# Kernel optimization log

Measured on AMD Instinct MI355X. Metric: run time of the kernel, lower is better.

Reference implementation:

```python
import jax, jax.numpy as jnp
import numpy as np

B, N, D, U = 128, 1024, 16, 128


def setup_inputs() -> dict:
    key = jax.random.key(0)
    ks = jax.random.split(key, 12)
    # get_normalized_adj: D^{-1/2} (A + I) D^{-1/2} on a sparse random graph
    A = (jax.random.uniform(ks[0], (N, N)) < 0.01).astype(jnp.float32)
    A = A + jnp.eye(N, dtype=jnp.float32)
    dinv = 1.0 / jnp.sqrt(A.sum(axis=1))
    support = dinv[:, None] * A * dinv[None, :]
    s = 0.05
    return {
        "x": jax.random.normal(ks[1], (2, B, N, D), jnp.float32),
        "hx": jax.random.normal(ks[2], (B, N * U), jnp.float32),
        "delta": jax.random.normal(ks[3], (B, N, D), jnp.float32),
        "support": support,
        "kernel_r": jax.random.normal(ks[4], (D + U, 2 * U), jnp.float32) * jnp.sqrt(2.0 / (D + U)),
        "kernel_c": jax.random.normal(ks[5], (D + U, U), jnp.float32) * jnp.sqrt(2.0 / (D + U)),
        "w_out": jax.random.normal(ks[6], (U + D, D), jnp.float32) * s,
        "b_out": jax.random.normal(ks[7], (D,), jnp.float32) * s,
        "w_basis": jax.random.normal(ks[8], (D, D), jnp.float32) * s,
        "b_basis": jax.random.normal(ks[9], (D,), jnp.float32) * s,
        "lam": jax.random.normal(ks[10], (1,), jnp.float32),
    }


def reference(x, hx, delta, support, kernel_r, kernel_c, w_out, b_out, w_basis, b_basis, lam):
    y_basis, y_res = x[0], x[1]                       # (B, N, D) each
    # speculative delta (add=True branch)
    delta_value = jax.nn.relu(y_res @ w_basis + b_basis)
    p_t = jax.nn.sigmoid(y_res + 0.5 * jnp.sqrt(jnp.abs(delta + 1e-9)))
    new_delta = lam * (2.0 * p_t - 1.0) * delta_value  # (B, N, D)

    hx3 = hx.reshape(B, N, U)

    def gconv(inp, state, kernel):
        # inp (B,N,D), state (B,N,U); diffusion_step == 1 Chebyshev pass
        xs = jnp.concatenate([inp, state], axis=-1)      # (B, N, D+U)
        xs = jnp.einsum('ij,bjl->bil', support, xs)      # diffusion over nodes
        return xs @ kernel                               # (B, N, out)

    value = jax.nn.sigmoid(gconv(y_basis, hx3, kernel_r))  # (B, N, 2U)
    r, u = value[..., :U], value[..., U:]
    c = jnp.tanh(gconv(y_basis, r * hx3, kernel_c))        # (B, N, U)

    u_flat = u.reshape(B, N * U)
    c_flat = c.reshape(B, N * U)
    new_state = hx * u_flat + c_flat * (1.0 - u_flat)      # (B, N*U)

    concat = jnp.concatenate([new_state.reshape(B, N, U), y_basis], axis=-1)
    o = concat @ w_out + b_out + new_delta                 # (B, N, D)
    return (o, new_state, new_delta)
```

## Files before the change

### kernel.cpp

```cpp
#include <hip/hip_runtime.h>
#include <cstdint>

#define B_ 128
#define N_ 1024
#define D_ 16
#define U_ 128
#define M_ (B_*N_)
#define K_ 144
#define KP 192
#define CAP 48

typedef unsigned short u16;
typedef unsigned int   u32;
typedef __attribute__((ext_vector_type(8))) short bf16x8;
typedef __attribute__((ext_vector_type(4))) float f32x4;

__device__ __forceinline__ float bf2f(u16 h){ return __uint_as_float(((u32)h) << 16); }
__device__ __forceinline__ u16 f2bf(float f){
    u32 u = __float_as_uint(f);
    return (u16)((u + 0x7FFFu + ((u >> 16) & 1u)) >> 16);
}
__device__ __forceinline__ float sig_(float x){ return 1.0f / (1.0f + __expf(-x)); }

__global__ void k_ell(const float* __restrict__ sup, float* __restrict__ vals,
                      int* __restrict__ cols, int* __restrict__ nnz)
{
    int wid  = (blockIdx.x * blockDim.x + threadIdx.x) >> 6;
    int lane = threadIdx.x & 63;
    if (wid >= N_) return;
    const float* row = sup + (size_t)wid * N_;
    int base = 0;
    for (int step = 0; step < N_/64; ++step){
        int j = step*64 + lane;
        float v = row[j];
        unsigned long long m = __ballot(v != 0.0f);
        int pos = base + __popcll(m & ((1ull << lane) - 1ull));
        if (v != 0.0f && pos < CAP){ vals[wid*CAP + pos] = v; cols[wid*CAP + pos] = j; }
        base += __popcll(m);
    }
    int cnt = base < CAP ? base : CAP;
    for (int p = cnt + lane; p < CAP; p += 64){
        vals[wid*CAP + p] = 0.0f;
        cols[wid*CAP + p] = 0;
    }
    if (lane == 0) nnz[wid] = (cnt + 3) & ~3;
}

__global__ void k_prep(const float* __restrict__ kr, const float* __restrict__ kc,
                       u16* __restrict__ wr_t, u16* __restrict__ wc_t)
{
    int t = blockIdx.x * 256 + threadIdx.x;
    if (t < 256*KP){
        int col = t / KP, k = t % KP;
        wr_t[t] = f2bf(k < K_ ? kr[k*256 + col] : 0.0f);
    } else {
        int q = t - 256*KP;
        int col = q / KP, k = q % KP;
        wc_t[q] = f2bf(k < K_ ? kc[k*128 + col] : 0.0f);
    }
}


#define GQB(JJ, WW)                                                            \
    {   uint2 hh = *(const uint2*)(s16 + (int)(JJ)*16 + cq*4);                 \
        float f0 = __uint_as_float(hh.x << 16);                                \
        float f1 = __uint_as_float(hh.x & 0xFFFF0000u);                        \
        float f2 = __uint_as_float(hh.y << 16);                                \
        float f3 = __uint_as_float(hh.y & 0xFFFF0000u);                        \
        acc.x = fmaf((WW), f0, acc.x); acc.y = fmaf((WW), f1, acc.y);          \
        acc.z = fmaf((WW), f2, acc.z); acc.w = fmaf((WW), f3, acc.w); }

#define GB(T0)                                                                 \
    {   float4 wv = *(const float4*)(vt + (T0));                               \
        int4   jv = *(const int4*)(ct + (T0));                                 \
        GQB(jv.x, wv.x); GQB(jv.y, wv.y); GQB(jv.z, wv.z); GQB(jv.w, wv.w); }

#define PACK8(PK, VA, VB)                                                      \
    uint4 PK; PK.x = (u32)f2bf((VA).x) | ((u32)f2bf((VA).y) << 16);            \
    PK.y = (u32)f2bf((VA).z) | ((u32)f2bf((VA).w) << 16);                      \
    PK.z = (u32)f2bf((VB).x) | ((u32)f2bf((VB).y) << 16);                      \
    PK.w = (u32)f2bf((VB).z) | ((u32)f2bf((VB).w) << 16);

__global__ __launch_bounds__(512, 8) void k_spmm1(
        const float* __restrict__ x, const float* __restrict__ hx,
        const float* __restrict__ vals, const int* __restrict__ cols,
        const int* __restrict__ nnz, u16* __restrict__ agg)
{
    __shared__ u16 s16[1024*16];
    const int chunk = blockIdx.x;
    const int b     = blockIdx.y;
    const int tid   = threadIdx.x;
    const int cb    = chunk * 16;

    for (int q = tid; q < 2048; q += 512){
        int row = q >> 1, part = q & 1;
        const float* src = (chunk == 0)
            ? &x[((size_t)((b<<10)+row))*16 + part*8]
            : &hx[((size_t)((b<<10)+row))*128 + (cb-16) + part*8];
        float4 va = *(const float4*)src;
        float4 vb = *(const float4*)(src + 4);
        PACK8(pk, va, vb)
        *(uint4*)(s16 + row*16 + part*8) = pk;
    }
    __syncthreads();

    for (int p = tid; p < 4096; p += 512){
        int node = p >> 2, cq = p & 3;
        int c = nnz[node];
        const float* vt = vals + node*CAP;
        const int*   ct = cols + node*CAP;
        float4 acc = make_float4(0.f,0.f,0.f,0.f);
        GB(0) GB(4) GB(8) GB(12)
        for (int t0 = 16; t0 < c; t0 += 4) GB(t0)
        size_t m = (size_t)(b<<10) + node;
        ushort4 pv; pv.x = f2bf(acc.x); pv.y = f2bf(acc.y);
        pv.z = f2bf(acc.z); pv.w = f2bf(acc.w);
        *(ushort4*)&agg[m*KP + cb + cq*4] = pv;
    }
}

__global__ __launch_bounds__(512, 8) void k_spmm2(
        const u16* __restrict__ value, const float* __restrict__ hx,
        const float* __restrict__ vals, const int* __restrict__ cols,
        const int* __restrict__ nnz, u16* __restrict__ agg)
{
    __shared__ u16 s16[1024*16];
    const int chunk = blockIdx.x;
    const int b     = blockIdx.y;
    const int tid   = threadIdx.x;
    const int cb    = chunk * 16;

    for (int q = tid; q < 2048; q += 512){
        int row = q >> 1, part = q & 1;
        size_t nb = (size_t)((b<<10)+row);
        int hxcol = cb + part*8;
        float4 h0 = *(const float4*)&hx[nb*128 + hxcol];
        float4 h1 = *(const float4*)&hx[nb*128 + hxcol + 4];
        ushort4 r0 = *(const ushort4*)&value[nb*256 + hxcol];
        ushort4 r1 = *(const ushort4*)&value[nb*256 + hxcol + 4];
        float4 va = make_float4(bf2f(r0.x)*h0.x, bf2f(r0.y)*h0.y,
                                bf2f(r0.z)*h0.z, bf2f(r0.w)*h0.w);
        float4 vb = make_float4(bf2f(r1.x)*h1.x, bf2f(r1.y)*h1.y,
                                bf2f(r1.z)*h1.z, bf2f(r1.w)*h1.w);
        PACK8(pk, va, vb)
        *(uint4*)(s16 + row*16 + part*8) = pk;
    }
    __syncthreads();

    for (int p = tid; p < 4096; p += 512){
        int node = p >> 2, cq = p & 3;
        int c = nnz[node];
        const float* vt = vals + node*CAP;
        const int*   ct = cols + node*CAP;
        float4 acc = make_float4(0.f,0.f,0.f,0.f);
        GB(0) GB(4) GB(8) GB(12)
        for (int t0 = 16; t0 < c; t0 += 4) GB(t0)
        size_t m = (size_t)(b<<10) + node;
        ushort4 pv; pv.x = f2bf(acc.x); pv.y = f2bf(acc.y);
        pv.z = f2bf(acc.z); pv.w = f2bf(acc.w);
        *(ushort4*)&agg[m*KP + D_ + cb + cq*4] = pv;
    }
}


#define GEMM_STAGE_A                                                           \
    _Pragma("unroll")                                                          \
    for (int i = 0; i < 4; ++i){                                               \
        int q = tid + i*256;                                                   \
        int r_ = q >> 3, sl = q & 7;                                           \
        uint4 v = {0,0,0,0};                                                   \
        if (kb + sl*8 < K_)                                                    \
            v = *(const uint4*)(agg + (size_t)(rb+r_)*KP + kb + sl*8);         \
        *(uint4*)(a_s + r_*72 + sl*8) = v;                                     \
    }

#define GEMM_STAGE_W                                                           \
    _Pragma("unroll")                                                          \
    for (int i = 0; i < 4; ++i){                                               \
        int q = tid + i*256;                                                   \
        int r_ = q >> 3, sl = q & 7;                                           \
        uint4 v = *(const uint4*)(wt + (size_t)(cb+r_)*KP + kb + sl*8);        \
        *(uint4*)(w_s + r_*72 + sl*8) = v;                                     \
    }

#define GEMM_CORE                                                              \
    for (int kb = 0; kb < KP; kb += 64){                                       \
        __syncthreads();                                                       \
        GEMM_STAGE_A                                                           \
        GEMM_STAGE_W                                                           \
        __syncthreads();                                                       \
        _Pragma("unroll")                                                      \
        for (int ks = 0; ks < 2; ++ks){                                        \
            bf16x8 af[4], bfv[4];                                              \
            _Pragma("unroll")                                                  \
            for (int f = 0; f < 4; ++f){                                       \
                af[f]  = *(const bf16x8*)(a_s + (wr + f*16 + lrow)*72 + ks*32 + lk); \
                bfv[f] = *(const bf16x8*)(w_s + (wc + f*16 + lrow)*72 + ks*32 + lk); \
            }                                                                  \
            _Pragma("unroll")                                                  \
            for (int fr = 0; fr < 4; ++fr)                                     \
                _Pragma("unroll")                                              \
                for (int fc = 0; fc < 4; ++fc)                                 \
                    acc[fr][fc] = __builtin_amdgcn_mfma_f32_16x16x32_bf16(     \
                        af[fr], bfv[fc], acc[fr][fc], 0, 0, 0);                \
        }                                                                      \
    }

__global__ __launch_bounds__(256) void k_gemm1(const u16* __restrict__ agg,
        const u16* __restrict__ wt, u16* __restrict__ value)
{
    __shared__ u16 a_s[128*72];
    __shared__ u16 w_s[128*72];
    const int rb = blockIdx.x * 128, cb = blockIdx.y * 128;
    const int tid = threadIdx.x;
    const int wid = tid >> 6, lane = tid & 63;
    const int wr = (wid >> 1) * 64, wc = (wid & 1) * 64;
    const int lrow = lane & 15, lk = (lane >> 4) * 8;
    f32x4 acc[4][4] = {};
    GEMM_CORE
    const int rg = (lane >> 4) * 4;
    #pragma unroll
    for (int fr = 0; fr < 4; ++fr)
        #pragma unroll
        for (int fc = 0; fc < 4; ++fc)
            #pragma unroll
            for (int j = 0; j < 4; ++j){
                int row = rb + wr + fr*16 + rg + j;
                int col = cb + wc + fc*16 + lrow;
                value[(size_t)row*256 + col] = f2bf(sig_(acc[fr][fc][j]));
            }
}

__global__ __launch_bounds__(256) void k_gemm2(const u16* __restrict__ agg,
        const u16* __restrict__ wt, const float* __restrict__ hx,
        const u16* value, float* ns_out)
{
    __shared__ u16 a_s[128*72];
    __shared__ u16 w_s[128*72];
    const int rb = blockIdx.x * 128, cb = 0;
    const int tid = threadIdx.x;
    const int wid = tid >> 6, lane = tid & 63;
    const int wr = (wid >> 1) * 64, wc = (wid & 1) * 64;
    const int lrow = lane & 15, lk = (lane >> 4) * 8;
    f32x4 acc[4][4] = {};
    GEMM_CORE
    const int rg = (lane >> 4) * 4;
    float ov[4][4][4];
    #pragma unroll
    for (int fr = 0; fr < 4; ++fr)
        #pragma unroll
        for (int fc = 0; fc < 4; ++fc)
            #pragma unroll
            for (int j = 0; j < 4; ++j){
                int row = rb + wr + fr*16 + rg + j;
                int col = wc + fc*16 + lrow;
                float u = bf2f(value[(size_t)row*256 + 128 + col]);
                float h = hx[(size_t)row*128 + col];
                float c = tanhf(acc[fr][fc][j]);
                ov[fr][fc][j] = h*u + c*(1.0f - u);
            }
    __syncthreads();
    #pragma unroll
    for (int fr = 0; fr < 4; ++fr)
        #pragma unroll
        for (int fc = 0; fc < 4; ++fc)
            #pragma unroll
            for (int j = 0; j < 4; ++j){
                int row = rb + wr + fr*16 + rg + j;
                int col = wc + fc*16 + lrow;
                ns_out[(size_t)row*128 + col] = ov[fr][fc][j];
            }
}

__global__ __launch_bounds__(256) void k_out(const float* __restrict__ ns,
        const float* __restrict__ x, const float* __restrict__ delta,
        const float* __restrict__ wo, const float* __restrict__ bo,
        const float* __restrict__ wb, const float* __restrict__ bb,
        const float* __restrict__ lam,
        float* __restrict__ o, float* __restrict__ nd_out)
{
    __shared__ float ns_s[64][132];
    __shared__ float yb_s[64][20];
    __shared__ float yr_s[64][20];
    __shared__ float w_s[144][16];
    __shared__ float wb_s[16][16];
    __shared__ float bo_s[16], bb_s[16];
    int rowbase = blockIdx.x * 64;
    int tid = threadIdx.x;
    const float* yr = x + (size_t)M_ * D_;
    #pragma unroll
    for (int jj = 0; jj < 8; ++jj){
        int q = tid + 256*jj;
        int row = q >> 5, c4 = (q & 31) * 4;
        *(float4*)&ns_s[row][c4] = *(const float4*)&ns[(size_t)(rowbase + row)*U_ + c4];
    }
    {
        int row = tid >> 2, c4 = (tid & 3) * 4;
        *(float4*)&yb_s[row][c4] = *(const float4*)&x[(size_t)(rowbase + row)*D_ + c4];
        *(float4*)&yr_s[row][c4] = *(const float4*)&yr[(size_t)(rowbase + row)*D_ + c4];
    }
    #pragma unroll
    for (int jj = 0; jj < 3; ++jj){
        int q = tid + 256*jj;
        if (q < 576){ int k = q >> 2, d4 = (q & 3) * 4;
            *(float4*)&w_s[k][d4] = *(const float4*)&wo[k*D_ + d4]; }
    }
    wb_s[tid >> 4][tid & 15] = wb[tid];
    if (tid < 16){ bo_s[tid] = bo[tid]; bb_s[tid] = bb[tid]; }
    __syncthreads();
    int row = tid >> 2, d0 = (tid & 3) * 4;
    float4 acc = make_float4(0.f,0.f,0.f,0.f);
    for (int k = 0; k < U_; ++k){
        float cs = ns_s[row][k];
        float4 w = *(const float4*)&w_s[k][d0];
        acc.x = fmaf(cs, w.x, acc.x); acc.y = fmaf(cs, w.y, acc.y);
        acc.z = fmaf(cs, w.z, acc.z); acc.w = fmaf(cs, w.w, acc.w);
    }
    #pragma unroll
    for (int k = 0; k < D_; ++k){
        float cs = yb_s[row][k];
        float4 w = *(const float4*)&w_s[U_ + k][d0];
        acc.x = fmaf(cs, w.x, acc.x); acc.y = fmaf(cs, w.y, acc.y);
        acc.z = fmaf(cs, w.z, acc.z); acc.w = fmaf(cs, w.w, acc.w);
    }
    float4 dacc = make_float4(bb_s[d0], bb_s[d0+1], bb_s[d0+2], bb_s[d0+3]);
    #pragma unroll
    for (int k = 0; k < D_; ++k){
        float yv = yr_s[row][k];
        float4 w = *(const float4*)&wb_s[k][d0];
        dacc.x = fmaf(yv, w.x, dacc.x); dacc.y = fmaf(yv, w.y, dacc.y);
        dacc.z = fmaf(yv, w.z, dacc.z); dacc.w = fmaf(yv, w.w, dacc.w);
    }
    size_t off = (size_t)(rowbase + row)*D_ + d0;
    float4 dl = *(const float4*)&delta[off];
    float lm = lam[0];
    float nd4[4];
    float yv4[4] = {yr_s[row][d0], yr_s[row][d0+1], yr_s[row][d0+2], yr_s[row][d0+3]};
    float dv4[4] = {fmaxf(dacc.x,0.f), fmaxf(dacc.y,0.f), fmaxf(dacc.z,0.f), fmaxf(dacc.w,0.f)};
    float dl4[4] = {dl.x, dl.y, dl.z, dl.w};
    #pragma unroll
    for (int j = 0; j < 4; ++j){
        float pt = sig_(yv4[j] + 0.5f * sqrtf(fabsf(dl4[j] + 1e-9f)));
        nd4[j] = lm * (2.0f * pt - 1.0f) * dv4[j];
    }
    float4 bov = *(const float4*)&bo_s[d0];
    float4 ov = make_float4(acc.x + bov.x + nd4[0], acc.y + bov.y + nd4[1],
                            acc.z + bov.z + nd4[2], acc.w + bov.w + nd4[3]);
    *(float4*)&nd_out[off] = make_float4(nd4[0], nd4[1], nd4[2], nd4[3]);
    *(float4*)&o[off] = ov;
}

extern "C" void kernel_launch(void* const* d_in, const int* in_sizes, int n_in,
                              void* d_out, int out_size, void* d_ws, size_t ws_size,
                              hipStream_t stream)
{
    const float* x        = (const float*)d_in[0];
    const float* hx       = (const float*)d_in[1];
    const float* delta    = (const float*)d_in[2];
    const float* support  = (const float*)d_in[3];
    const float* kernel_r = (const float*)d_in[4];
    const float* kernel_c = (const float*)d_in[5];
    const float* w_out    = (const float*)d_in[6];
    const float* b_out    = (const float*)d_in[7];
    const float* w_basis  = (const float*)d_in[8];
    const float* b_basis  = (const float*)d_in[9];
    const float* lam      = (const float*)d_in[10];

    float* out = (float*)d_out;
    float* o   = out;
    float* ns  = out + 2097152;
    float* nd  = out + 18874368;
    u16*   value = (u16*)ns;

    char* ws = (char*)d_ws;
    float* ell_vals = (float*)ws;
    int*   ell_cols = (int*)(ws + 1024*CAP*4);
    int*   ell_nnz  = (int*)(ws + 2*1024*CAP*4);
    u16*   agg      = (u16*)(ws + (1 << 20));
    u16*   wr_t     = (u16*)(ws + (1 << 20) + (size_t)M_*KP*2);
    u16*   wc_t     = wr_t + 256*KP;

    k_ell  <<<256, 256, 0, stream>>>(support, ell_vals, ell_cols, ell_nnz);
    k_prep <<<(256*KP + 128*KP)/256, 256, 0, stream>>>(kernel_r, kernel_c, wr_t, wc_t);
    k_spmm1<<<dim3(9,128), 512, 0, stream>>>(x, hx, ell_vals, ell_cols, ell_nnz, agg);
    k_gemm1<<<dim3(M_/128, 2), 256, 0, stream>>>(agg, wr_t, value);
    k_spmm2<<<dim3(8,128), 512, 0, stream>>>(value, hx, ell_vals, ell_cols, ell_nnz, agg);
    k_gemm2<<<M_/128, 256, 0, stream>>>(agg, wc_t, hx, value, ns);
    k_out  <<<M_/64, 256, 0, stream>>>(ns, x, delta, w_out, b_out,
                                       w_basis, b_basis, lam, o, nd);
}
```

Baseline: 244.1 us.

## Fuse output projection into gemm2 epilogue and cover both gate halves per gemm1 block

```diff
diff --git a/kernel.cpp b/kernel.cpp
--- a/kernel.cpp
+++ b/kernel.cpp
@@ -162,89 +162,130 @@
     }
 }
 
-
-#define GEMM_STAGE_A                                                           \
-    _Pragma("unroll")                                                          \
-    for (int i = 0; i < 4; ++i){                                               \
-        int q = tid + i*256;                                                   \
-        int r_ = q >> 3, sl = q & 7;                                           \
-        uint4 v = {0,0,0,0};                                                   \
-        if (kb + sl*8 < K_)                                                    \
-            v = *(const uint4*)(agg + (size_t)(rb+r_)*KP + kb + sl*8);         \
-        *(uint4*)(a_s + r_*72 + sl*8) = v;                                     \
-    }
-
-#define GEMM_STAGE_W                                                           \
-    _Pragma("unroll")                                                          \
-    for (int i = 0; i < 4; ++i){                                               \
-        int q = tid + i*256;                                                   \
-        int r_ = q >> 3, sl = q & 7;                                           \
-        uint4 v = *(const uint4*)(wt + (size_t)(cb+r_)*KP + kb + sl*8);        \
-        *(uint4*)(w_s + r_*72 + sl*8) = v;                                     \
-    }
-
-#define GEMM_CORE                                                              \
-    for (int kb = 0; kb < KP; kb += 64){                                       \
-        __syncthreads();                                                       \
-        GEMM_STAGE_A                                                           \
-        GEMM_STAGE_W                                                           \
-        __syncthreads();                                                       \
-        _Pragma("unroll")                                                      \
-        for (int ks = 0; ks < 2; ++ks){                                        \
-            bf16x8 af[4], bfv[4];                                              \
-            _Pragma("unroll")                                                  \
-            for (int f = 0; f < 4; ++f){                                       \
-                af[f]  = *(const bf16x8*)(a_s + (wr + f*16 + lrow)*72 + ks*32 + lk); \
-                bfv[f] = *(const bf16x8*)(w_s + (wc + f*16 + lrow)*72 + ks*32 + lk); \
-            }                                                                  \
-            _Pragma("unroll")                                                  \
-            for (int fr = 0; fr < 4; ++fr)                                     \
-                _Pragma("unroll")                                              \
-                for (int fc = 0; fc < 4; ++fc)                                 \
-                    acc[fr][fc] = __builtin_amdgcn_mfma_f32_16x16x32_bf16(     \
-                        af[fr], bfv[fc], acc[fr][fc], 0, 0, 0);                \
-        }                                                                      \
-    }
-
 __global__ __launch_bounds__(256) void k_gemm1(const u16* __restrict__ agg,
         const u16* __restrict__ wt, u16* __restrict__ value)
 {
-    __shared__ u16 a_s[128*72];
+    __shared__ u16 a_s[128*168];
     __shared__ u16 w_s[128*72];
-    const int rb = blockIdx.x * 128, cb = blockIdx.y * 128;
+    const int rb = blockIdx.x * 128;
     const int tid = threadIdx.x;
     const int wid = tid >> 6, lane = tid & 63;
     const int wr = (wid >> 1) * 64, wc = (wid & 1) * 64;
     const int lrow = lane & 15, lk = (lane >> 4) * 8;
-    f32x4 acc[4][4] = {};
-    GEMM_CORE
     const int rg = (lane >> 4) * 4;
-    #pragma unroll
-    for (int fr = 0; fr < 4; ++fr)
-        #pragma unroll
-        for (int fc = 0; fc < 4; ++fc)
-            #pragma unroll
-            for (int j = 0; j < 4; ++j){
-                int row = rb + wr + fr*16 + rg + j;
-                int col = cb + wc + fc*16 + lrow;
-                value[(size_t)row*256 + col] = f2bf(sig_(acc[fr][fc][j]));
+
+    for (int q = tid; q < 128*21; q += 256){
+        int r_ = q / 21, seg = q % 21;
+        uint4 v = {0,0,0,0};
+        if (seg < 18) v = *(const uint4*)(agg + (size_t)(rb+r_)*KP + seg*8);
+        *(uint4*)(a_s + r_*168 + seg*8) = v;
+    }
+
+    for (int half = 0; half < 2; ++half){
+        const int cbase = half * 128;
+        f32x4 acc[4][4] = {};
+        for (int kb = 0; kb < KP; kb += 64){
+            __syncthreads();
+            #pragma unroll
+            for (int i2 = 0; i2 < 4; ++i2){
+                int q = tid + i2*256;
+                int r_ = q >> 3, sl = q & 7;
+                uint4 v = *(const uint4*)(wt + (size_t)(cbase+r_)*KP + kb + sl*8);
+                *(uint4*)(w_s + r_*72 + sl*8) = v;
             }
+            __syncthreads();
+            #pragma unroll
+            for (int ks = 0; ks < 2; ++ks){
+                bf16x8 af[4], bfv[4];
+                #pragma unroll
+                for (int f = 0; f < 4; ++f){
+                    af[f]  = *(const bf16x8*)(a_s + (wr + f*16 + lrow)*168 + kb + ks*32 + lk);
+                    bfv[f] = *(const bf16x8*)(w_s + (wc + f*16 + lrow)*72 + ks*32 + lk);
+                }
+                #pragma unroll
+                for (int fr = 0; fr < 4; ++fr)
+                    #pragma unroll
+                    for (int fc = 0; fc < 4; ++fc)
+                        acc[fr][fc] = __builtin_amdgcn_mfma_f32_16x16x32_bf16(
+                            af[fr], bfv[fc], acc[fr][fc], 0, 0, 0);
+            }
+        }
+        #pragma unroll
+        for (int fr = 0; fr < 4; ++fr)
+            #pragma unroll
+            for (int fc = 0; fc < 4; ++fc)
+                #pragma unroll
+                for (int j = 0; j < 4; ++j){
+                    int row = rb + wr + fr*16 + rg + j;
+                    int col = cbase + wc + fc*16 + lrow;
+                    value[(size_t)row*256 + col] = f2bf(sig_(acc[fr][fc][j]));
+                }
+    }
 }
 
 __global__ __launch_bounds__(256) void k_gemm2(const u16* __restrict__ agg,
         const u16* __restrict__ wt, const float* __restrict__ hx,
-        const u16* value, float* ns_out)
-{
-    __shared__ u16 a_s[128*72];
-    __shared__ u16 w_s[128*72];
-    const int rb = blockIdx.x * 128, cb = 0;
+        const u16* value, float* ns_out,
+        const float* __restrict__ x, const float* __restrict__ delta,
+        const float* __restrict__ wo, const float* __restrict__ bo,
+        const float* __restrict__ wb, const float* __restrict__ bb,
+        const float* __restrict__ lam,
+        float* __restrict__ o, float* __restrict__ nd_out)
+{
+    __shared__ u16 smem[128*72*2];
+    __shared__ float wo_s[144*16];
+    __shared__ float wb_s[16*16];
+    __shared__ float bo_s[16], bb_s[16];
+    u16* a_s = smem;
+    u16* w_s = smem + 128*72;
+    const int rb = blockIdx.x * 128;
     const int tid = threadIdx.x;
     const int wid = tid >> 6, lane = tid & 63;
     const int wr = (wid >> 1) * 64, wc = (wid & 1) * 64;
     const int lrow = lane & 15, lk = (lane >> 4) * 8;
+    const int rg = (lane >> 4) * 4;
+
+    for (int q = tid; q < 144*16; q += 256) wo_s[q] = wo[q];
+    wb_s[tid & 255] = wb[tid & 255];
+    if (tid < 16){ bo_s[tid] = bo[tid]; bb_s[tid] = bb[tid]; }
+
     f32x4 acc[4][4] = {};
-    GEMM_CORE
-    const int rg = (lane >> 4) * 4;
+    for (int kb = 0; kb < KP; kb += 64){
+        __syncthreads();
+        #pragma unroll
+        for (int i2 = 0; i2 < 4; ++i2){
+            int q = tid + i2*256;
+            int r_ = q >> 3, sl = q & 7;
+            uint4 v = {0,0,0,0};
+            if (kb + sl*8 < K_)
+                v = *(const uint4*)(agg + (size_t)(rb+r_)*KP + kb + sl*8);
+            *(uint4*)(a_s + r_*72 + sl*8) = v;
+        }
+        #pragma unroll
+        for (int i2 = 0; i2 < 4; ++i2){
+            int q = tid + i2*256;
+            int r_ = q >> 3, sl = q & 7;
+            uint4 v = *(const uint4*)(wt + (size_t)r_*KP + kb + sl*8);
+            *(uint4*)(w_s + r_*72 + sl*8) = v;
+        }
+        __syncthreads();
+        #pragma unroll
+        for (int ks = 0; ks < 2; ++ks){
+            bf16x8 af[4], bfv[4];
+            #pragma unroll
+            for (int f = 0; f < 4; ++f){
+                af[f]  = *(const bf16x8*)(a_s + (wr + f*16 + lrow)*72 + ks*32 + lk);
+                bfv[f] = *(const bf16x8*)(w_s + (wc + f*16 + lrow)*72 + ks*32 + lk);
+            }
+            #pragma unroll
+            for (int fr = 0; fr < 4; ++fr)
+                #pragma unroll
+                for (int fc = 0; fc < 4; ++fc)
+                    acc[fr][fc] = __builtin_amdgcn_mfma_f32_16x16x32_bf16(
+                        af[fr], bfv[fc], acc[fr][fc], 0, 0, 0);
+        }
+    }
+
     float ov[4][4][4];
     #pragma unroll
     for (int fr = 0; fr < 4; ++fr)
@@ -260,94 +301,80 @@
                 ov[fr][fc][j] = h*u + c*(1.0f - u);
             }
     __syncthreads();
+    u16* ns_lds = smem;
     #pragma unroll
     for (int fr = 0; fr < 4; ++fr)
         #pragma unroll
         for (int fc = 0; fc < 4; ++fc)
             #pragma unroll
             for (int j = 0; j < 4; ++j){
-                int row = rb + wr + fr*16 + rg + j;
+                int r_loc = wr + fr*16 + rg + j;
                 int col = wc + fc*16 + lrow;
-                ns_out[(size_t)row*128 + col] = ov[fr][fc][j];
+                float v = ov[fr][fc][j];
+                ns_out[(size_t)(rb + r_loc)*128 + col] = v;
+                ns_lds[r_loc*140 + col] = f2bf(v);
             }
-}
-
-__global__ __launch_bounds__(256) void k_out(const float* __restrict__ ns,
-        const float* __restrict__ x, const float* __restrict__ delta,
-        const float* __restrict__ wo, const float* __restrict__ bo,
-        const float* __restrict__ wb, const float* __restrict__ bb,
-        const float* __restrict__ lam,
-        float* __restrict__ o, float* __restrict__ nd_out)
-{
-    __shared__ float ns_s[64][132];
-    __shared__ float yb_s[64][20];
-    __shared__ float yr_s[64][20];
-    __shared__ float w_s[144][16];
-    __shared__ float wb_s[16][16];
-    __shared__ float bo_s[16], bb_s[16];
-    int rowbase = blockIdx.x * 64;
-    int tid = threadIdx.x;
+    __syncthreads();
+
     const float* yr = x + (size_t)M_ * D_;
+    float lm = lam[0];
     #pragma unroll
-    for (int jj = 0; jj < 8; ++jj){
-        int q = tid + 256*jj;
-        int row = q >> 5, c4 = (q & 31) * 4;
-        *(float4*)&ns_s[row][c4] = *(const float4*)&ns[(size_t)(rowbase + row)*U_ + c4];
-    }
-    {
-        int row = tid >> 2, c4 = (tid & 3) * 4;
-        *(float4*)&yb_s[row][c4] = *(const float4*)&x[(size_t)(rowbase + row)*D_ + c4];
-        *(float4*)&yr_s[row][c4] = *(const float4*)&yr[(size_t)(rowbase + row)*D_ + c4];
-    }
-    #pragma unroll
-    for (int jj = 0; jj < 3; ++jj){
-        int q = tid + 256*jj;
-        if (q < 576){ int k = q >> 2, d4 = (q & 3) * 4;
-            *(float4*)&w_s[k][d4] = *(const float4*)&wo[k*D_ + d4]; }
-    }
-    wb_s[tid >> 4][tid & 15] = wb[tid];
-    if (tid < 16){ bo_s[tid] = bo[tid]; bb_s[tid] = bb[tid]; }
-    __syncthreads();
-    int row = tid >> 2, d0 = (tid & 3) * 4;
-    float4 acc = make_float4(0.f,0.f,0.f,0.f);
-    for (int k = 0; k < U_; ++k){
-        float cs = ns_s[row][k];
-        float4 w = *(const float4*)&w_s[k][d0];
-        acc.x = fmaf(cs, w.x, acc.x); acc.y = fmaf(cs, w.y, acc.y);
-        acc.z = fmaf(cs, w.z, acc.z); acc.w = fmaf(cs, w.w, acc.w);
-    }
-    #pragma unroll
-    for (int k = 0; k < D_; ++k){
-        float cs = yb_s[row][k];
-        float4 w = *(const float4*)&w_s[U_ + k][d0];
-        acc.x = fmaf(cs, w.x, acc.x); acc.y = fmaf(cs, w.y, acc.y);
-        acc.z = fmaf(cs, w.z, acc.z); acc.w = fmaf(cs, w.w, acc.w);
-    }
-    float4 dacc = make_float4(bb_s[d0], bb_s[d0+1], bb_s[d0+2], bb_s[d0+3]);
-    #pragma unroll
-    for (int k = 0; k < D_; ++k){
-        float yv = yr_s[row][k];
-        float4 w = *(const float4*)&wb_s[k][d0];
-        dacc.x = fmaf(yv, w.x, dacc.x); dacc.y = fmaf(yv, w.y, dacc.y);
-        dacc.z = fmaf(yv, w.z, dacc.z); dacc.w = fmaf(yv, w.w, dacc.w);
-    }
-    size_t off = (size_t)(rowbase + row)*D_ + d0;
-    float4 dl = *(const float4*)&delta[off];
-    float lm = lam[0];
-    float nd4[4];
-    float yv4[4] = {yr_s[row][d0], yr_s[row][d0+1], yr_s[row][d0+2], yr_s[row][d0+3]};
-    float dv4[4] = {fmaxf(dacc.x,0.f), fmaxf(dacc.y,0.f), fmaxf(dacc.z,0.f), fmaxf(dacc.w,0.f)};
-    float dl4[4] = {dl.x, dl.y, dl.z, dl.w};
-    #pragma unroll
-    for (int j = 0; j < 4; ++j){
-        float pt = sig_(yv4[j] + 0.5f * sqrtf(fabsf(dl4[j] + 1e-9f)));
-        nd4[j] = lm * (2.0f * pt - 1.0f) * dv4[j];
-    }
-    float4 bov = *(const float4*)&bo_s[d0];
-    float4 ov = make_float4(acc.x + bov.x + nd4[0], acc.y + bov.y + nd4[1],
-                            acc.z + bov.z + nd4[2], acc.w + bov.w + nd4[3]);
-    *(float4*)&nd_out[off] = make_float4(nd4[0], nd4[1], nd4[2], nd4[3]);
-    *(float4*)&o[off] = ov;
+    for (int it = 0; it < 2; ++it){
+        int item = tid + it*256;
+        int row = item >> 2, d0 = (item & 3) * 4;
+        size_t grow = (size_t)(rb + row);
+        float a0 = bo_s[d0], a1 = bo_s[d0+1], a2 = bo_s[d0+2], a3 = bo_s[d0+3];
+        const u16* nr = ns_lds + row*140;
+        for (int c = 0; c < 128; c += 4){
+            uint2 hh = *(const uint2*)(nr + c);
+            float n0 = __uint_as_float(hh.x << 16);
+            float n1 = __uint_as_float(hh.x & 0xFFFF0000u);
+            float n2 = __uint_as_float(hh.y << 16);
+            float n3 = __uint_as_float(hh.y & 0xFFFF0000u);
+            const float* w0 = wo_s + c*16 + d0;
+            a0 = fmaf(n0, w0[0],  a0); a1 = fmaf(n0, w0[1],  a1);
+            a2 = fmaf(n0, w0[2],  a2); a3 = fmaf(n0, w0[3],  a3);
+            a0 = fmaf(n1, w0[16], a0); a1 = fmaf(n1, w0[17], a1);
+            a2 = fmaf(n1, w0[18], a2); a3 = fmaf(n1, w0[19], a3);
+            a0 = fmaf(n2, w0[32], a0); a1 = fmaf(n2, w0[33], a1);
+            a2 = fmaf(n2, w0[34], a2); a3 = fmaf(n2, w0[35], a3);
+            a0 = fmaf(n3, w0[48], a0); a1 = fmaf(n3, w0[49], a1);
+            a2 = fmaf(n3, w0[50], a2); a3 = fmaf(n3, w0[51], a3);
+        }
+        float ybv[16], yrv[16];
+        #pragma unroll
+        for (int s = 0; s < 4; ++s){
+            float4 vb = *(const float4*)&x[grow*D_ + s*4];
+            float4 vr = *(const float4*)&yr[grow*D_ + s*4];
+            ybv[s*4+0]=vb.x; ybv[s*4+1]=vb.y; ybv[s*4+2]=vb.z; ybv[s*4+3]=vb.w;
+            yrv[s*4+0]=vr.x; yrv[s*4+1]=vr.y; yrv[s*4+2]=vr.z; yrv[s*4+3]=vr.w;
+        }
+        float b0 = bb_s[d0], b1 = bb_s[d0+1], b2 = bb_s[d0+2], b3 = bb_s[d0+3];
+        #pragma unroll
+        for (int k = 0; k < D_; ++k){
+            const float* w1 = wo_s + (U_ + k)*16 + d0;
+            float yv = ybv[k];
+            a0 = fmaf(yv, w1[0], a0); a1 = fmaf(yv, w1[1], a1);
+            a2 = fmaf(yv, w1[2], a2); a3 = fmaf(yv, w1[3], a3);
+            const float* w2 = wb_s + k*16 + d0;
+            float rv = yrv[k];
+            b0 = fmaf(rv, w2[0], b0); b1 = fmaf(rv, w2[1], b1);
+            b2 = fmaf(rv, w2[2], b2); b3 = fmaf(rv, w2[3], b3);
+        }
+        size_t off = grow*D_ + d0;
+        float4 dl = *(const float4*)&delta[off];
+        float dv[4] = {fmaxf(b0,0.f), fmaxf(b1,0.f), fmaxf(b2,0.f), fmaxf(b3,0.f)};
+        float dl4[4] = {dl.x, dl.y, dl.z, dl.w};
+        float nd4[4];
+        #pragma unroll
+        for (int j = 0; j < 4; ++j){
+            float pt = sig_(yrv[d0+j] + 0.5f * sqrtf(fabsf(dl4[j] + 1e-9f)));
+            nd4[j] = lm * (2.0f * pt - 1.0f) * dv[j];
+        }
+        *(float4*)&nd_out[off] = make_float4(nd4[0], nd4[1], nd4[2], nd4[3]);
+        *(float4*)&o[off] = make_float4(a0 + nd4[0], a1 + nd4[1],
+                                        a2 + nd4[2], a3 + nd4[3]);
+    }
 }
 
 extern "C" void kernel_launch(void* const* d_in, const int* in_sizes, int n_in,
@@ -374,8 +401,8 @@
 
     char* ws = (char*)d_ws;
     float* ell_vals = (float*)ws;
-    int*   ell_cols = (int*)(ws + 1024*CAP*4);
-    int*   ell_nnz  = (int*)(ws + 2*1024*CAP*4);
+    int*   ell_cols = (int*)(ws + 196608);
+    int*   ell_nnz  = (int*)(ws + 393216);
     u16*   agg      = (u16*)(ws + (1 << 20));
     u16*   wr_t     = (u16*)(ws + (1 << 20) + (size_t)M_*KP*2);
     u16*   wc_t     = wr_t + 256*KP;
@@ -383,9 +410,9 @@
     k_ell  <<<256, 256, 0, stream>>>(support, ell_vals, ell_cols, ell_nnz);
     k_prep <<<(256*KP + 128*KP)/256, 256, 0, stream>>>(kernel_r, kernel_c, wr_t, wc_t);
     k_spmm1<<<dim3(9,128), 512, 0, stream>>>(x, hx, ell_vals, ell_cols, ell_nnz, agg);
-    k_gemm1<<<dim3(M_/128, 2), 256, 0, stream>>>(agg, wr_t, value);
+    k_gemm1<<<1024, 256, 0, stream>>>(agg, wr_t, value);
     k_spmm2<<<dim3(8,128), 512, 0, stream>>>(value, hx, ell_vals, ell_cols, ell_nnz, agg);
-    k_gemm2<<<M_/128, 256, 0, stream>>>(agg, wc_t, hx, value, ns);
-    k_out  <<<M_/64, 256, 0, stream>>>(ns, x, delta, w_out, b_out,
-                                       w_basis, b_basis, lam, o, nd);
-}
+    k_gemm2<<<1024, 256, 0, stream>>>(agg, wc_t, hx, value, ns,
+                                      x, delta, w_out, b_out,
+                                      w_basis, b_basis, lam, o, nd);
+}
```

After: 488.4 us. 100% more time.
